# Kernel tuning notes

Measured on AMD Instinct MI355X. Metric: run time of the kernel, lower is better.

Reference implementation:

```python
import jax, jax.numpy as jnp
import numpy as np

B, C, R = 100000, 64, 128

def setup_inputs() -> dict:
    key = jax.random.key(0)
    k1, k2, k3 = jax.random.split(key, 3)
    return {
        "compressed_vectors": jax.random.normal(k1, (B, C, 3), dtype=jnp.float32),
        "W1": jax.random.normal(k2, (C, 32), dtype=jnp.float32) * (1.0 / np.sqrt(C)),
        "b1": jnp.zeros((32,), dtype=jnp.float32),
        "W2": jax.random.normal(k3, (32, R * C), dtype=jnp.float32) * (1.0 / np.sqrt(32)),
        "b2": jnp.zeros((R * C,), dtype=jnp.float32),
    }

def reference(compressed_vectors, W1, b1, W2, b2):
    # scalar invariants: L2 norm over Cartesian axis -> [B, C]
    scalar_invariants = jnp.linalg.norm(compressed_vectors, axis=-1)
    # tiny MLP: C -> 32 -> R*C
    h = jax.nn.relu(scalar_invariants @ W1 + b1)
    scalar_weights = (h @ W2 + b2).reshape(-1, R, C)  # [B, R, C]
    # outer product of vectors: [B, C, 3, 3]
    rank2_tensors = jnp.einsum('bci,bcj->bcij', compressed_vectors, compressed_vectors)
    # weighted bilinear contraction over channels: [B, R, 3, 3]
    reconstructed_tensors = jnp.einsum('brc,bcij->brij', scalar_weights, rank2_tensors)
    return reconstructed_tensors
```

## Files before the change

kernel.cpp:

```cpp
#include <hip/hip_runtime.h>
#include <hip/hip_bf16.h>


#define NB 16
#define RT 8

typedef float f32x4 __attribute__((ext_vector_type(4)));
typedef __bf16 bf16x8 __attribute__((ext_vector_type(8)));

static __device__ __forceinline__ unsigned short bf_bits(float f) {
  __hip_bfloat16 h = __float2bfloat16(f);
  return *reinterpret_cast<const unsigned short*>(&h);
}
static __device__ __forceinline__ unsigned int pack_bf2(float a, float b) {
  return (unsigned int)bf_bits(a) | ((unsigned int)bf_bits(b) << 16);
}

__global__ void prep_w2t(const float* __restrict__ W2, unsigned short* __restrict__ w2t) {
  int rc = blockIdx.x * 256 + threadIdx.x;
  unsigned int u[16];
#pragma unroll
  for (int kp = 0; kp < 16; ++kp) {
    float a = W2[(size_t)(2 * kp) * 8192 + rc];
    float b = W2[(size_t)(2 * kp + 1) * 8192 + rc];
    u[kp] = pack_bf2(a, b);
  }
  unsigned int* dst = reinterpret_cast<unsigned int*>(w2t + (size_t)rc * 32);
#pragma unroll
  for (int j = 0; j < 16; ++j) dst[j] = u[j];
}

__global__ __launch_bounds__(256, 4)
void erl_main(const float* __restrict__ v, const float* __restrict__ W1,
              const float* __restrict__ b1, const float* __restrict__ b2,
              const unsigned short* __restrict__ w2t, float* __restrict__ out) {
  __shared__ __align__(16) unsigned short W_lds[NB * 584];
  __shared__ __align__(16) unsigned short M_lds[NB * 6 * 72];
  __shared__ __align__(16) float O_sh[NB * RT * 6];
  __shared__ __align__(16) unsigned short h_lds[NB * 32];
  __shared__ __align__(16) float s_lds[NB * 65];

  const int t = threadIdx.x;
  const int b0 = blockIdx.x * NB;
  const int lane = t & 63;
  const int wid = t >> 6;
  const int x = lane >> 4;
  const int col = lane & 15;

#pragma unroll
  for (int j = 0; j < (NB * 64) / 256; ++j) {
    int p = t + j * 256;
    int b = p >> 6, c = p & 63;
    const float* vp = v + ((size_t)(b0 + b) * 64 + c) * 3;
    float vx = vp[0], vy = vp[1], vz = vp[2];
    s_lds[b * 65 + c] = sqrtf(vx * vx + vy * vy + vz * vz);
    unsigned short* mp = &M_lds[b * 6 * 72 + c];
    mp[0 * 72] = bf_bits(vx * vx);
    mp[1 * 72] = bf_bits(vy * vy);
    mp[2 * 72] = bf_bits(vz * vz);
    mp[3 * 72] = bf_bits(vx * vy);
    mp[4 * 72] = bf_bits(vx * vz);
    mp[5 * 72] = bf_bits(vy * vz);
  }
  __syncthreads();

#pragma unroll
  for (int j = 0; j < (NB * 32) / 256; ++j) {
    int idx = t + j * 256;
    int b = idx >> 5, k = idx & 31;
    float acc = b1[k];
    for (int c = 0; c < 64; ++c)
      acc = fmaf(s_lds[b * 65 + c], W1[c * 32 + k], acc);
    h_lds[b * 32 + k] = bf_bits(fmaxf(acc, 0.f));
  }
  __syncthreads();

  bf16x8 hfrag = *reinterpret_cast<const bf16x8*>(&h_lds[col * 32 + x * 8]);

  for (int rt = 0; rt < 128 / RT; ++rt) {
#pragma unroll
    for (int half = 0; half < 2; ++half) {
      bf16x8 af[4];
      f32x4 acc1[4];
#pragma unroll
      for (int i = 0; i < 4; ++i) {
        int tile = wid * 8 + half * 4 + i;
        int rcg = rt * 512 + tile * 16;
        af[i] = *reinterpret_cast<const bf16x8*>(&w2t[(size_t)(rcg + col) * 32 + x * 8]);
        acc1[i] = *reinterpret_cast<const f32x4*>(&b2[rcg + x * 4]);
      }
#pragma unroll
      for (int i = 0; i < 4; ++i) {
        acc1[i] = __builtin_amdgcn_mfma_f32_16x16x32_bf16(af[i], hfrag, acc1[i], 0, 0, 0);
        int rcl = (wid * 8 + half * 4 + i) * 16 + x * 4;
        int r = rcl >> 6, c = rcl & 63;
        unsigned int* wp = reinterpret_cast<unsigned int*>(&W_lds[col * 584 + r * 72 + c]);
        wp[0] = pack_bf2(acc1[i][0], acc1[i][1]);
        wp[1] = pack_bf2(acc1[i][2], acc1[i][3]);
      }
    }
    __syncthreads();

#pragma unroll
    for (int i = 0; i < 4; ++i) {
      int b = wid * 4 + i;
      int rr = col & 7;
      int ss = (col < 6) ? col : 5;
      f32x4 acc2 = {0.f, 0.f, 0.f, 0.f};
#pragma unroll
      for (int ch = 0; ch < 2; ++ch) {
        bf16x8 a2 = *reinterpret_cast<const bf16x8*>(&W_lds[b * 584 + rr * 72 + ch * 32 + x * 8]);
        bf16x8 m2 = *reinterpret_cast<const bf16x8*>(&M_lds[(b * 6 + ss) * 72 + ch * 32 + x * 8]);
        acc2 = __builtin_amdgcn_mfma_f32_16x16x32_bf16(a2, m2, acc2, 0, 0, 0);
      }
      if (x < 2 && col < 6) {
#pragma unroll
        for (int q = 0; q < 4; ++q)
          O_sh[b * 48 + (x * 4 + q) * 6 + col] = acc2[q];
      }
    }
    __syncthreads();

    for (int i = t; i < NB * RT * 9; i += 256) {
      int b = i / 72;
      int rem = i - b * 72;
      int r = rem / 9;
      int e = rem - r * 9;
      int ei = e / 3, ej = e - ei * 3;
      int s = (ei == ej) ? ei : (2 + ei + ej);
      out[((size_t)(b0 + b) * 128 + rt * RT + r) * 9 + e] = O_sh[b * 48 + r * 6 + s];
    }
  }
}

extern "C" void kernel_launch(void* const* d_in, const int* in_sizes, int n_in,
                              void* d_out, int out_size, void* d_ws, size_t ws_size,
                              hipStream_t stream) {
  const float* v  = (const float*)d_in[0];
  const float* W1 = (const float*)d_in[1];
  const float* b1 = (const float*)d_in[2];
  const float* W2 = (const float*)d_in[3];
  const float* b2 = (const float*)d_in[4];
  float* out = (float*)d_out;

  unsigned short* w2t = (unsigned short*)d_ws;

  prep_w2t<<<32, 256, 0, stream>>>(W2, w2t);
  erl_main<<<100000 / NB, 256, 0, stream>>>(v, W1, b1, b2, w2t, out);
}
```

Measured before the change: 366.7 us.

## Hold outer-product fragments in registers and store MFMA results directly to output

Builds the rank-2 outer-product B-operand fragments in registers, covering all 9 components instead of 6 symmetric ones, so the M_lds buffer goes away. The second MFMA's results are written straight to global memory, which removes the O_sh staging buffer, a barrier-free scatter loop with integer divisions, and its LDS traffic. W1 is staged in LDS, the first MLP layer is vectorised, and shared memory is aliased into one pool to cut LDS use and allow higher occupancy. The costs are more registers for the fragments and direct global stores with a 9-float stride that coalesce less well.

```diff
diff --git a/kernel.cpp b/kernel.cpp
--- a/kernel.cpp
+++ b/kernel.cpp
@@ -34,11 +34,11 @@
 void erl_main(const float* __restrict__ v, const float* __restrict__ W1,
               const float* __restrict__ b1, const float* __restrict__ b2,
               const unsigned short* __restrict__ w2t, float* __restrict__ out) {
-  __shared__ __align__(16) unsigned short W_lds[NB * 584];
-  __shared__ __align__(16) unsigned short M_lds[NB * 6 * 72];
-  __shared__ __align__(16) float O_sh[NB * RT * 6];
-  __shared__ __align__(16) unsigned short h_lds[NB * 32];
-  __shared__ __align__(16) float s_lds[NB * 65];
+  __shared__ __align__(16) char smem[24064];
+  unsigned short* W_lds = reinterpret_cast<unsigned short*>(smem);
+  float* W1_lds = reinterpret_cast<float*>(smem);
+  float* s_lds = reinterpret_cast<float*>(smem + 18688);
+  unsigned short* h_lds = reinterpret_cast<unsigned short*>(smem + 23040);
 
   const int t = threadIdx.x;
   const int b0 = blockIdx.x * NB;
@@ -47,89 +47,117 @@
   const int x = lane >> 4;
   const int col = lane & 15;
 
+  {
+    const f32x4* w1v = reinterpret_cast<const f32x4*>(W1);
+    f32x4* w1d = reinterpret_cast<f32x4*>(W1_lds);
+    w1d[t] = w1v[t];
+    w1d[t + 256] = w1v[t + 256];
+  }
 #pragma unroll
-  for (int j = 0; j < (NB * 64) / 256; ++j) {
+  for (int j = 0; j < 4; ++j) {
     int p = t + j * 256;
     int b = p >> 6, c = p & 63;
     const float* vp = v + ((size_t)(b0 + b) * 64 + c) * 3;
     float vx = vp[0], vy = vp[1], vz = vp[2];
-    s_lds[b * 65 + c] = sqrtf(vx * vx + vy * vy + vz * vz);
-    unsigned short* mp = &M_lds[b * 6 * 72 + c];
-    mp[0 * 72] = bf_bits(vx * vx);
-    mp[1 * 72] = bf_bits(vy * vy);
-    mp[2 * 72] = bf_bits(vz * vz);
-    mp[3 * 72] = bf_bits(vx * vy);
-    mp[4 * 72] = bf_bits(vx * vz);
-    mp[5 * 72] = bf_bits(vy * vz);
+    s_lds[b * 68 + c] = sqrtf(vx * vx + vy * vy + vz * vz);
+  }
+
+  const int seff = (col < 9) ? col : 8;
+  const int ei = seff / 3;
+  const int ej = seff - ei * 3;
+  bf16x8 mfr[4][2];
+#pragma unroll
+  for (int i = 0; i < 4; ++i) {
+    int b = wid * 4 + i;
+#pragma unroll
+    for (int ch = 0; ch < 2; ++ch) {
+      const float* vb = v + ((size_t)(b0 + b) * 64 + ch * 32 + x * 8) * 3;
+      union { f32x4 q[6]; float f[24]; } u;
+#pragma unroll
+      for (int l = 0; l < 6; ++l) u.q[l] = reinterpret_cast<const f32x4*>(vb)[l];
+      bf16x8 fr;
+#pragma unroll
+      for (int e = 0; e < 8; ++e) {
+        float vx = u.f[e * 3 + 0], vy = u.f[e * 3 + 1], vz = u.f[e * 3 + 2];
+        float pa = (ei == 0) ? vx : ((ei == 1) ? vy : vz);
+        float pb = (ej == 0) ? vx : ((ej == 1) ? vy : vz);
+        fr[e] = (__bf16)(pa * pb);
+      }
+      mfr[i][ch] = fr;
+    }
   }
   __syncthreads();
 
+  {
+    int b = t >> 4, kk = t & 15;
+    float a0 = b1[kk], a1 = b1[kk + 16];
+    const f32x4* srow = reinterpret_cast<const f32x4*>(s_lds + b * 68);
 #pragma unroll
-  for (int j = 0; j < (NB * 32) / 256; ++j) {
-    int idx = t + j * 256;
-    int b = idx >> 5, k = idx & 31;
-    float acc = b1[k];
-    for (int c = 0; c < 64; ++c)
-      acc = fmaf(s_lds[b * 65 + c], W1[c * 32 + k], acc);
-    h_lds[b * 32 + k] = bf_bits(fmaxf(acc, 0.f));
+    for (int c4 = 0; c4 < 16; ++c4) {
+      f32x4 sv = srow[c4];
+#pragma unroll
+      for (int uu = 0; uu < 4; ++uu) {
+        int c = c4 * 4 + uu;
+        a0 = fmaf(sv[uu], W1_lds[c * 32 + kk], a0);
+        a1 = fmaf(sv[uu], W1_lds[c * 32 + kk + 16], a1);
+      }
+    }
+    h_lds[b * 32 + kk] = bf_bits(fmaxf(a0, 0.f));
+    h_lds[b * 32 + kk + 16] = bf_bits(fmaxf(a1, 0.f));
   }
   __syncthreads();
 
   bf16x8 hfrag = *reinterpret_cast<const bf16x8*>(&h_lds[col * 32 + x * 8]);
 
+  const unsigned short* ap0 = w2t + (size_t)wid * 4096 + col * 32 + x * 8;
+  const unsigned short* ap1 = ap0 + 2048;
+  const float* b2p = b2 + wid * 128 + x * 4;
+  const int w_widx = col * 584 + wid * 144 + x * 4;
+  const int w_ridx = wid * 4 * 584 + (col & 7) * 72 + x * 8;
+  float* op[4];
+#pragma unroll
+  for (int i = 0; i < 4; ++i)
+    op[i] = out + (size_t)(b0 + wid * 4 + i) * 1152 + x * 36 + col;
+  const bool do_store = (x < 2) && (col < 9);
+
   for (int rt = 0; rt < 128 / RT; ++rt) {
 #pragma unroll
     for (int half = 0; half < 2; ++half) {
+      const unsigned short* ap = half ? ap1 : ap0;
       bf16x8 af[4];
       f32x4 acc1[4];
 #pragma unroll
       for (int i = 0; i < 4; ++i) {
-        int tile = wid * 8 + half * 4 + i;
-        int rcg = rt * 512 + tile * 16;
-        af[i] = *reinterpret_cast<const bf16x8*>(&w2t[(size_t)(rcg + col) * 32 + x * 8]);
-        acc1[i] = *reinterpret_cast<const f32x4*>(&b2[rcg + x * 4]);
+        af[i] = *reinterpret_cast<const bf16x8*>(ap + i * 512);
+        acc1[i] = *reinterpret_cast<const f32x4*>(b2p + half * 64 + i * 16);
       }
 #pragma unroll
       for (int i = 0; i < 4; ++i) {
         acc1[i] = __builtin_amdgcn_mfma_f32_16x16x32_bf16(af[i], hfrag, acc1[i], 0, 0, 0);
-        int rcl = (wid * 8 + half * 4 + i) * 16 + x * 4;
-        int r = rcl >> 6, c = rcl & 63;
-        unsigned int* wp = reinterpret_cast<unsigned int*>(&W_lds[col * 584 + r * 72 + c]);
+        unsigned int* wp = reinterpret_cast<unsigned int*>(&W_lds[w_widx + half * 72 + i * 16]);
         wp[0] = pack_bf2(acc1[i][0], acc1[i][1]);
         wp[1] = pack_bf2(acc1[i][2], acc1[i][3]);
       }
     }
+    ap0 += 16384; ap1 += 16384; b2p += 512;
     __syncthreads();
 
 #pragma unroll
     for (int i = 0; i < 4; ++i) {
-      int b = wid * 4 + i;
-      int rr = col & 7;
-      int ss = (col < 6) ? col : 5;
       f32x4 acc2 = {0.f, 0.f, 0.f, 0.f};
 #pragma unroll
       for (int ch = 0; ch < 2; ++ch) {
-        bf16x8 a2 = *reinterpret_cast<const bf16x8*>(&W_lds[b * 584 + rr * 72 + ch * 32 + x * 8]);
-        bf16x8 m2 = *reinterpret_cast<const bf16x8*>(&M_lds[(b * 6 + ss) * 72 + ch * 32 + x * 8]);
-        acc2 = __builtin_amdgcn_mfma_f32_16x16x32_bf16(a2, m2, acc2, 0, 0, 0);
+        bf16x8 a2 = *reinterpret_cast<const bf16x8*>(&W_lds[w_ridx + i * 584 + ch * 32]);
+        acc2 = __builtin_amdgcn_mfma_f32_16x16x32_bf16(a2, mfr[i][ch], acc2, 0, 0, 0);
       }
-      if (x < 2 && col < 6) {
+      if (do_store) {
+        float* p = op[i];
 #pragma unroll
-        for (int q = 0; q < 4; ++q)
-          O_sh[b * 48 + (x * 4 + q) * 6 + col] = acc2[q];
+        for (int q = 0; q < 4; ++q) p[q * 9] = acc2[q];
       }
+      op[i] += 72;
     }
     __syncthreads();
-
-    for (int i = t; i < NB * RT * 9; i += 256) {
-      int b = i / 72;
-      int rem = i - b * 72;
-      int r = rem / 9;
-      int e = rem - r * 9;
-      int ei = e / 3, ej = e - ei * 3;
-      int s = (ei == ej) ? ei : (2 + ei + ej);
-      out[((size_t)(b0 + b) * 128 + rt * RT + r) * 9 + e] = O_sh[b * 48 + r * 6 + s];
-    }
   }
 }
 
```

After: 403.8 us. +10.1%, slower.
